# Kernel optimization log

Measured on AMD Instinct MI355X. Metric: run time of the kernel, lower is better.

## Reference

```python
import jax, jax.numpy as jnp
from jax import lax
import numpy as np

B, T, DM = 4, 2048, 768
LYR, DI, N, DC, R = 2, 1536, 64, 4, 48  # layers, d_inner, d_state, d_conv, dt_rank
EPS = 1e-5


def _silu(x):
    return x * jax.nn.sigmoid(x)


def _layernorm(x, w, b):
    m = x.mean(-1, keepdims=True)
    v = ((x - m) ** 2).mean(-1, keepdims=True)
    return (x - m) * lax.rsqrt(v + EPS) * w + b


def _mamba(x, W_in, Wc, bc, W_x, W_dt, b_dt, a_log, Dp, W_out):
    # x: [B,T,DM]; standard Mamba block (mamba_ssm), bias-free in/out projections
    b, t, _ = x.shape
    d_inner = Dp.shape[0]
    n = a_log.shape[1]
    r = W_dt.shape[1]
    xz = jnp.einsum('btd,ed->bte', x, W_in)      # [B,T,2*DI]
    u, z = jnp.split(xz, 2, axis=-1)
    # causal depthwise conv along T
    u_c = lax.conv_general_dilated(u.transpose(0, 2, 1), Wc[:, None, :], (1,),
                                   [(DC - 1, 0)], dimension_numbers=('NCH', 'OIH', 'NCH'),
                                   feature_group_count=d_inner)
    u_c = _silu((u_c + bc[None, :, None]).transpose(0, 2, 1))  # [B,T,DI]
    proj = jnp.einsum('btd,ed->bte', u_c, W_x)   # [B,T,R+2N]
    dt, Bm, Cm = proj[..., :r], proj[..., r:r + n], proj[..., r + n:]
    delta = jax.nn.softplus(jnp.einsum('btr,dr->btd', dt, W_dt) + b_dt)  # [B,T,DI]
    A = -jnp.exp(a_log)                           # [DI,N]

    def step(h, inp):
        d_t, u_t, B_t, C_t = inp                 # [B,DI],[B,DI],[B,N],[B,N]
        h = h * jnp.exp(d_t[..., None] * A) + d_t[..., None] * B_t[:, None, :] * u_t[..., None]
        return h, jnp.einsum('bdn,bn->bd', h, C_t)

    h0 = jnp.zeros((b, d_inner, n), x.dtype)
    _, ys = lax.scan(step, h0, (delta.transpose(1, 0, 2), u_c.transpose(1, 0, 2),
                                Bm.transpose(1, 0, 2), Cm.transpose(1, 0, 2)))
    y = ys.transpose(1, 0, 2) + u_c * Dp         # [B,T,DI]
    y = y * _silu(z)
    return jnp.einsum('btd,od->bto', y, W_out)   # [B,T,DM]


def setup_inputs() -> dict:
    key = jax.random.key(0)
    ks = jax.random.split(key, 12)
    s = 0.02
    A0 = jnp.log(jnp.arange(1, N + 1, dtype=jnp.float32))  # standard S4D-real init
    return {
        'x': jax.random.normal(ks[0], (B, T, DM), jnp.float32),
        'mask': jnp.ones((B, T), jnp.float32),
        'film_gamma': 1.0 + 0.1 * jax.random.normal(ks[1], (LYR, B, T, DM), jnp.float32),
        'film_beta': 0.1 * jax.random.normal(ks[2], (LYR, B, T, DM), jnp.float32),
        'in_proj_w': s * jax.random.normal(ks[3], (LYR, 2 * DI, DM), jnp.float32),
        'conv_w': s * jax.random.normal(ks[4], (LYR, DI, DC), jnp.float32),
        'conv_b': s * jax.random.normal(ks[5], (LYR, DI), jnp.float32),
        'x_proj_w': s * jax.random.normal(ks[6], (LYR, R + 2 * N, DI), jnp.float32),
        'dt_proj_w': s * jax.random.normal(ks[7], (LYR, DI, R), jnp.float32),
        'dt_proj_b': jnp.full((LYR, DI), -4.6, jnp.float32),  # softplus -> dt ~ 0.01
        'A_log': jnp.broadcast_to(A0, (LYR, DI, N)).copy(),
        'D': jnp.ones((LYR, DI), jnp.float32),
        'out_proj_w': s * jax.random.normal(ks[8], (LYR, DM, DI), jnp.float32),
        'ln_w': jnp.ones((LYR, DM), jnp.float32),
        'ln_b': jnp.zeros((LYR, DM), jnp.float32),
    }


def reference(x, mask, film_gamma, film_beta, in_proj_w, conv_w, conv_b, x_proj_w,
              dt_proj_w, dt_proj_b, A_log, D, out_proj_w, ln_w, ln_b):
    x = x * mask[..., None]
    for i in range(in_proj_w.shape[0]):
        residual = x
        h = _mamba(x, in_proj_w[i], conv_w[i], conv_b[i], x_proj_w[i], dt_proj_w[i],
                   dt_proj_b[i], A_log[i], D[i], out_proj_w[i])
        h = _layernorm(h, ln_w[i], ln_b[i])
        h = film_gamma[i] * h + film_beta[i]
        x = h + residual  # dropout is identity in eval mode
    return x
```

## Files before the change

kernel.cpp:

```cpp
#include <hip/hip_runtime.h>
#include <hip/hip_bf16.h>
#include <math.h>

#define BBv   4
#define TTv   2048
#define DMv   768
#define DIv   1536
#define NSv   64
#define DCv   4
#define RRv   48
#define PJW   176
#define NLYR  2
#define MROWS (BBv * TTv)

#define TBLK  16
#define LDST  68

typedef __attribute__((ext_vector_type(8))) short short8;
typedef __attribute__((ext_vector_type(4))) float f32x4;

__device__ __forceinline__ __hip_bfloat16 f2bf(float f) { return __float2bfloat16(f); }
__device__ __forceinline__ float bf2f(__hip_bfloat16 h) { return __bfloat162float(h); }
__device__ __forceinline__ float bits2f(unsigned u) {
    union { unsigned u; float f; } c; c.u = u; return c.f;
}

__global__ void cvt_weights_kernel(const float* __restrict__ w_in,
                                   const float* __restrict__ w_xp,
                                   const float* __restrict__ w_dt,
                                   const float* __restrict__ w_out,
                                   __hip_bfloat16* __restrict__ o_in,
                                   __hip_bfloat16* __restrict__ o_xp,
                                   __hip_bfloat16* __restrict__ o_dt,
                                   __hip_bfloat16* __restrict__ o_out)
{
    const size_t S1 = (size_t)NLYR * 2 * DIv * DMv;
    const size_t S2 = (size_t)NLYR * PJW * DIv;
    const size_t S3 = (size_t)NLYR * DIv * RRv;
    const size_t S4 = (size_t)NLYR * DMv * DIv;
    const size_t total = S1 + S2 + S3 + S4;
    for (size_t i = (size_t)blockIdx.x * blockDim.x + threadIdx.x; i < total;
         i += (size_t)gridDim.x * blockDim.x) {
        if (i < S1)                o_in[i]            = f2bf(w_in[i]);
        else if (i < S1 + S2)      o_xp[i - S1]       = f2bf(w_xp[i - S1]);
        else if (i < S1 + S2 + S3) o_dt[i - S1 - S2]  = f2bf(w_dt[i - S1 - S2]);
        else                       o_out[i - S1 - S2 - S3] = f2bf(w_out[i - S1 - S2 - S3]);
    }
}

__global__ void mask_x_kernel(const float* __restrict__ x,
                              const float* __restrict__ mask,
                              float* __restrict__ x_cur,
                              __hip_bfloat16* __restrict__ x_bf)
{
    size_t idx = (size_t)blockIdx.x * 256 + threadIdx.x;
    if (idx >= (size_t)MROWS * DMv) return;
    size_t row = idx / DMv;
    float v = x[idx] * mask[row];
    x_cur[idx] = v;
    x_bf[idx] = f2bf(v);
}

__global__ __launch_bounds__(256)
void transpose_bf16(const ushort* __restrict__ in, ushort* __restrict__ out,
                    int R, int C)
{
    __shared__ ushort s[64][68];
    const int tx = threadIdx.x & 15;
    const int ty = threadIdx.x >> 4;
    const size_t r0 = (size_t)blockIdx.y * 64;
    const size_t c0 = (size_t)blockIdx.x * 64;
    #pragma unroll
    for (int i = 0; i < 4; ++i) {
        int r = ty + 16 * i;
        ushort4 v = *(const ushort4*)(in + (r0 + r) * C + c0 + tx * 4);
        *(ushort4*)&s[r][tx * 4] = v;
    }
    __syncthreads();
    #pragma unroll
    for (int i = 0; i < 4; ++i) {
        int c = ty + 16 * i;
        ushort4 v;
        v.x = s[tx * 4 + 0][c];
        v.y = s[tx * 4 + 1][c];
        v.z = s[tx * 4 + 2][c];
        v.w = s[tx * 4 + 3][c];
        *(ushort4*)(out + (c0 + c) * R + r0 + tx * 4) = v;
    }
}

template<int EPI>
__global__ __launch_bounds__(256)
void gemm_nt(const __hip_bfloat16* __restrict__ A, int lda,
             const __hip_bfloat16* __restrict__ Bw, int ldb,
             float* __restrict__ Cf, __hip_bfloat16* __restrict__ Ch,
             __hip_bfloat16* __restrict__ ChT, int ldc,
             const float* __restrict__ bias, int M, int N, int K)
{
    __shared__ __align__(16) __hip_bfloat16 sA[64 * 48];
    __shared__ __align__(16) __hip_bfloat16 sB[64 * 48];
    const int tid = threadIdx.x;
    const int m0 = blockIdx.y * 64;
    const int n0 = blockIdx.x * 64;
    const int w = tid >> 6, lane = tid & 63;
    const int wr = (w >> 1) << 5;
    const int wc = (w & 1) << 5;
    const int lr = lane & 15, lk = lane >> 4;
    const int srow = tid >> 2;
    const int scol = (tid & 3) << 3;
    f32x4 acc[2][2] = {};
    const bool bvalid = (n0 + srow) < N;

    for (int k0 = 0; k0 < K; k0 += 32) {
        uint4 av = {0u, 0u, 0u, 0u}, bv = {0u, 0u, 0u, 0u};
        const bool kv = (k0 + scol) < K;
        if (kv)
            av = *(const uint4*)(A + (size_t)(m0 + srow) * lda + (k0 + scol));
        if (kv && bvalid)
            bv = *(const uint4*)(Bw + (size_t)(n0 + srow) * ldb + (k0 + scol));
        *(uint4*)(sA + srow * 48 + scol) = av;
        *(uint4*)(sB + srow * 48 + scol) = bv;
        __syncthreads();
        short8 af0 = *(const short8*)(sA + (wr + lr) * 48 + (lk << 3));
        short8 af1 = *(const short8*)(sA + (wr + 16 + lr) * 48 + (lk << 3));
        short8 bf0 = *(const short8*)(sB + (wc + lr) * 48 + (lk << 3));
        short8 bf1 = *(const short8*)(sB + (wc + 16 + lr) * 48 + (lk << 3));
        acc[0][0] = __builtin_amdgcn_mfma_f32_16x16x32_bf16(af0, bf0, acc[0][0], 0, 0, 0);
        acc[0][1] = __builtin_amdgcn_mfma_f32_16x16x32_bf16(af0, bf1, acc[0][1], 0, 0, 0);
        acc[1][0] = __builtin_amdgcn_mfma_f32_16x16x32_bf16(af1, bf0, acc[1][0], 0, 0, 0);
        acc[1][1] = __builtin_amdgcn_mfma_f32_16x16x32_bf16(af1, bf1, acc[1][1], 0, 0, 0);
        __syncthreads();
    }
    #pragma unroll
    for (int i = 0; i < 2; ++i) {
        #pragma unroll
        for (int j = 0; j < 2; ++j) {
            const int col = n0 + wc + (j << 4) + lr;
            const int rowb = m0 + wr + (i << 4) + (lk << 2);
            if (col >= N) continue;
            if constexpr (EPI == 0) {
                #pragma unroll
                for (int r = 0; r < 4; ++r)
                    Cf[(size_t)(rowb + r) * ldc + col] = acc[i][j][r];
            } else if constexpr (EPI == 2) {
                f32x4 sp;
                #pragma unroll
                for (int r = 0; r < 4; ++r) {
                    float xx = acc[i][j][r] + bias[col];
                    sp[r] = fmaxf(xx, 0.f) + log1pf(__expf(-fabsf(xx)));
                }
                *(f32x4*)(Cf + (size_t)col * MROWS + rowb) = sp;
            } else if constexpr (EPI == 3) {
                #pragma unroll
                for (int r = 0; r < 4; ++r) {
                    const int row = rowb + r;
                    float v = acc[i][j][r];
                    if (col < RRv)
                        Ch[(size_t)row * RRv + col] = f2bf(v);
                    else if (col < RRv + NSv)
                        Cf[(size_t)row * 128 + 2 * (col - RRv)] = v;
                    else
                        Cf[(size_t)row * 128 + 2 * (col - RRv - NSv) + 1] = v;
                }
            } else {
                if (col < DIv) {
                    #pragma unroll
                    for (int r = 0; r < 4; ++r)
                        Ch[(size_t)(rowb + r) * DIv + col] = f2bf(acc[i][j][r]);
                } else {
                    union { ushort4 v; __hip_bfloat16 h[4]; } zz;
                    #pragma unroll
                    for (int r = 0; r < 4; ++r) zz.h[r] = f2bf(acc[i][j][r]);
                    *(ushort4*)(ChT + (size_t)(col - DIv) * MROWS + rowb) = zz.v;
                }
            }
        }
    }
}

__global__ void conv_silu_kernel(const __hip_bfloat16* __restrict__ u_raw,
                                 const float* __restrict__ Wc,
                                 const float* __restrict__ bc,
                                 __hip_bfloat16* __restrict__ uc)
{
    size_t idx = (size_t)blockIdx.x * 256 + threadIdx.x;
    if (idx >= (size_t)MROWS * DIv) return;
    int d = (int)(idx % DIv);
    size_t row = idx / DIv;
    int t = (int)(row % TTv);
    float acc = bc[d];
    #pragma unroll
    for (int k = 0; k < DCv; ++k) {
        int tt = t - (DCv - 1) + k;
        if (tt >= 0)
            acc += Wc[d * DCv + k] *
                   bf2f(u_raw[(row - (DCv - 1) + k) * DIv + d]);
    }
    float s = acc / (1.f + __expf(-acc));
    uc[idx] = f2bf(s);
}

__global__ __launch_bounds__(256, 6)
void scan_kernel(const float* __restrict__ deltaT,
                 const __hip_bfloat16* __restrict__ ucT,
                 const __hip_bfloat16* __restrict__ zT,
                 const float* __restrict__ BC,
                 const float* __restrict__ a_log,
                 const float* __restrict__ Dp,
                 __hip_bfloat16* __restrict__ yT)
{
    __shared__ __align__(16) float vbuf[4 * TBLK * LDST];
    const int w = threadIdx.x >> 6;
    const int lane = threadIdx.x & 63;
    const int wid = blockIdx.x * 4 + w;
    const int b = __builtin_amdgcn_readfirstlane(wid / DIv);
    const int d = __builtin_amdgcn_readfirstlane(wid % DIv);
    const size_t bT = (size_t)b * TTv;
    const size_t dbase = (size_t)d * MROWS + bT;

    const float A2 = -__expf(a_log[(size_t)d * NSv + lane]) * 1.44269504088896f;
    const float Dd = Dp[d];

    const float4* dp4 = (const float4*)(deltaT + dbase);
    const uint4*  up4 = (const uint4*)(ucT + dbase);
    const float*  bcp = BC + bT * 128 + 2 * lane;
    float* vb = vbuf + w * (TBLK * LDST);

    float4 dA[2], dB[2];
    uint4  uu[2];
    float2 bc[2][8];

    dA[0] = dp4[0]; dB[0] = dp4[1]; uu[0] = up4[0];
    #pragma unroll
    for (int i = 0; i < 8; ++i)
        bc[0][i] = *(const float2*)(bcp + i * 128);

    float h = 0.f;
    for (int t0 = 0; t0 < TTv; t0 += TBLK) {
        #pragma unroll
        for (int q = 0; q < 2; ++q) {
            const int c = (t0 >> 3) + q;
            dA[q ^ 1] = dp4[(c + 1) * 2];
            dB[q ^ 1] = dp4[(c + 1) * 2 + 1];
            uu[q ^ 1] = up4[c + 1];
            const float* bq = bcp + (size_t)(c + 1) * 1024;
            #pragma unroll
            for (int i = 0; i < 8; ++i)
                bc[q ^ 1][i] = *(const float2*)(bq + i * 128);

            float dl[8] = { dA[q].x, dA[q].y, dA[q].z, dA[q].w,
                            dB[q].x, dB[q].y, dB[q].z, dB[q].w };
            float uf[8];
            uf[0] = bits2f(uu[q].x << 16); uf[1] = bits2f(uu[q].x & 0xffff0000u);
            uf[2] = bits2f(uu[q].y << 16); uf[3] = bits2f(uu[q].y & 0xffff0000u);
            uf[4] = bits2f(uu[q].z << 16); uf[5] = bits2f(uu[q].z & 0xffff0000u);
            uf[6] = bits2f(uu[q].w << 16); uf[7] = bits2f(uu[q].w & 0xffff0000u);

            #pragma unroll
            for (int i = 0; i < 8; ++i) {
                const float dlt = dl[i];
                const float e = exp2f(dlt * A2);
                h = fmaf(h, e, (dlt * uf[i]) * bc[q][i].x);
                vb[(q * 8 + i) * LDST + lane] = h * bc[q][i].y;
            }
        }
        __asm__ volatile("s_waitcnt lgkmcnt(0)" ::: "memory");
        const int r = lane & 15;
        const int cb = (lane >> 4) << 4;
        const float* vr = vb + r * LDST + cb;
        f32x4 a = *(const f32x4*)(vr);
        a += *(const f32x4*)(vr + 4);
        a += *(const f32x4*)(vr + 8);
        a += *(const f32x4*)(vr + 12);
        float s = a[0] + a[1] + a[2] + a[3];
        s += __shfl_xor(s, 16, 64);
        s += __shfl_xor(s, 32, 64);
        if (lane < 16) {
            const size_t g = dbase + t0 + r;
            const float u = bf2f(ucT[g]);
            const float z = bf2f(zT[g]);
            float yv = s + u * Dd;
            yv *= z / (1.f + __expf(-z));
            yT[g] = f2bf(yv);
        }
    }
}

__global__ __launch_bounds__(256)
void ln_film_res_kernel(const float* __restrict__ h,
                        const float* __restrict__ xres,
                        const float* __restrict__ lw,
                        const float* __restrict__ lb,
                        const float* __restrict__ gamma,
                        const float* __restrict__ beta,
                        float* __restrict__ xout,
                        __hip_bfloat16* __restrict__ xbf)
{
    __shared__ float sm[4];
    const int row = blockIdx.x;
    const int tid = threadIdx.x;
    const int w = tid >> 6, lane = tid & 63;
    const float* hr = h + (size_t)row * DMv;
    float v0 = hr[tid], v1 = hr[tid + 256], v2 = hr[tid + 512];

    float s = v0 + v1 + v2;
    #pragma unroll
    for (int off = 32; off > 0; off >>= 1) s += __shfl_xor(s, off, 64);
    if (lane == 0) sm[w] = s;
    __syncthreads();
    float mean = (sm[0] + sm[1] + sm[2] + sm[3]) * (1.f / DMv);
    __syncthreads();

    float d0 = v0 - mean, d1 = v1 - mean, d2 = v2 - mean;
    float vs = d0 * d0 + d1 * d1 + d2 * d2;
    #pragma unroll
    for (int off = 32; off > 0; off >>= 1) vs += __shfl_xor(vs, off, 64);
    if (lane == 0) sm[w] = vs;
    __syncthreads();
    float var = (sm[0] + sm[1] + sm[2] + sm[3]) * (1.f / DMv);
    float rstd = rsqrtf(var + 1e-5f);

    const float dv[3] = {d0, d1, d2};
    #pragma unroll
    for (int e = 0; e < 3; ++e) {
        int c = tid + e * 256;
        size_t gi = (size_t)row * DMv + c;
        float ln = dv[e] * rstd * lw[c] + lb[c];
        float f = gamma[gi] * ln + beta[gi];
        float o = f + xres[gi];
        xout[gi] = o;
        xbf[gi] = f2bf(o);
    }
}

extern "C" void kernel_launch(void* const* d_in, const int* in_sizes, int n_in,
                              void* d_out, int out_size, void* d_ws, size_t ws_size,
                              hipStream_t stream)
{
    const float* x     = (const float*)d_in[0];
    const float* mask  = (const float*)d_in[1];
    const float* fg    = (const float*)d_in[2];
    const float* fb    = (const float*)d_in[3];
    const float* w_in  = (const float*)d_in[4];
    const float* w_c   = (const float*)d_in[5];
    const float* b_c   = (const float*)d_in[6];
    const float* w_xp  = (const float*)d_in[7];
    const float* w_dt  = (const float*)d_in[8];
    const float* b_dt  = (const float*)d_in[9];
    const float* a_log = (const float*)d_in[10];
    const float* Dp    = (const float*)d_in[11];
    const float* w_out = (const float*)d_in[12];
    const float* ln_w  = (const float*)d_in[13];
    const float* ln_b  = (const float*)d_in[14];

    char* p = (char*)d_ws;
    __hip_bfloat16* uraw_yT = (__hip_bfloat16*)p; p += (size_t)MROWS * DIv * 2;
    __hip_bfloat16* uc_y    = (__hip_bfloat16*)p; p += (size_t)MROWS * DIv * 2;
    __hip_bfloat16* ucT     = (__hip_bfloat16*)p; p += (size_t)DIv * MROWS * 2 + 4096;
    __hip_bfloat16* zT      = (__hip_bfloat16*)p; p += (size_t)DIv * MROWS * 2;
    __hip_bfloat16* x_bf    = (__hip_bfloat16*)p; p += (size_t)MROWS * DMv * 2;
    __hip_bfloat16* dtA_bf  = (__hip_bfloat16*)p; p += (size_t)MROWS * RRv * 2;
    __hip_bfloat16* wbf_in  = (__hip_bfloat16*)p; p += (size_t)NLYR * 2 * DIv * DMv * 2;
    __hip_bfloat16* wbf_xp  = (__hip_bfloat16*)p; p += (size_t)NLYR * PJW * DIv * 2;
    __hip_bfloat16* wbf_dt  = (__hip_bfloat16*)p; p += (size_t)NLYR * DIv * RRv * 2;
    __hip_bfloat16* wbf_out = (__hip_bfloat16*)p; p += (size_t)NLYR * DMv * DIv * 2;
    float* BCbuf  = (float*)p; p += (size_t)MROWS * 128 * 4 + 8192;
    float* deltaT = (float*)p; p += (size_t)DIv * MROWS * 4 + 4096;
    float* x_cur  = (float*)p; p += (size_t)MROWS * DMv * 4;
    float* hbuf   = deltaT;

    cvt_weights_kernel<<<4096, 256, 0, stream>>>(w_in, w_xp, w_dt, w_out,
                                                 wbf_in, wbf_xp, wbf_dt, wbf_out);
    mask_x_kernel<<<(MROWS * DMv) / 256, 256, 0, stream>>>(x, mask, x_cur, x_bf);

    for (int L = 0; L < NLYR; ++L) {
        const __hip_bfloat16* WinL  = wbf_in  + (size_t)L * 2 * DIv * DMv;
        const __hip_bfloat16* WxpL  = wbf_xp  + (size_t)L * PJW * DIv;
        const __hip_bfloat16* WdtL  = wbf_dt  + (size_t)L * DIv * RRv;
        const __hip_bfloat16* WoutL = wbf_out + (size_t)L * DMv * DIv;

        gemm_nt<4><<<dim3(2 * DIv / 64, MROWS / 64), 256, 0, stream>>>(
            x_bf, DMv, WinL, DMv, nullptr, uraw_yT, zT, 0, nullptr,
            MROWS, 2 * DIv, DMv);

        conv_silu_kernel<<<(MROWS * DIv) / 256, 256, 0, stream>>>(
            uraw_yT, w_c + (size_t)L * DIv * DCv, b_c + (size_t)L * DIv, uc_y);

        transpose_bf16<<<dim3(DIv / 64, MROWS / 64), 256, 0, stream>>>(
            (const ushort*)uc_y, (ushort*)ucT, MROWS, DIv);

        gemm_nt<3><<<dim3((PJW + 63) / 64, MROWS / 64), 256, 0, stream>>>(
            uc_y, DIv, WxpL, DIv, BCbuf, dtA_bf, nullptr, 0, nullptr,
            MROWS, PJW, DIv);

        gemm_nt<2><<<dim3(DIv / 64, MROWS / 64), 256, 0, stream>>>(
            dtA_bf, RRv, WdtL, RRv, deltaT, nullptr, nullptr, 0,
            b_dt + (size_t)L * DIv, MROWS, DIv, RRv);

        scan_kernel<<<(BBv * DIv) / 4, 256, 0, stream>>>(
            deltaT, ucT, zT, BCbuf,
            a_log + (size_t)L * DIv * NSv, Dp + (size_t)L * DIv, uraw_yT);

        transpose_bf16<<<dim3(MROWS / 64, DIv / 64), 256, 0, stream>>>(
            (const ushort*)uraw_yT, (ushort*)uc_y, DIv, MROWS);

        gemm_nt<0><<<dim3(DMv / 64, MROWS / 64), 256, 0, stream>>>(
            uc_y, DIv, WoutL, DIv, hbuf, nullptr, nullptr, DMv, nullptr,
            MROWS, DMv, DIv);

        float* xo = (L == NLYR - 1) ? (float*)d_out : x_cur;
        ln_film_res_kernel<<<MROWS, 256, 0, stream>>>(
            hbuf, x_cur, ln_w + (size_t)L * DMv, ln_b + (size_t)L * DMv,
            fg + (size_t)L * MROWS * DMv, fb + (size_t)L * MROWS * DMv,
            xo, x_bf);
    }
}
```

Before: 1.588 ms.

## Enlarge GEMM tile to 128x64 and use hardware exp2/rcp intrinsics

The bf16 MFMA GEMM goes from a 64x64 to a 128x64 block tile. Each wave now computes 32x64 with 8 accumulators, and the LDS stride is padded to 56 to reduce bank conflicts. Operand reuse per K step is higher and fewer blocks load B. Separately, the sigmoid/SiLU and exp computations in the conv, scan init, scan recurrence and scan gating switch to the raw amdgcn exp2/rcp builtins, which cost fewer instructions but are slightly less accurate. Doubling the tile halves the grid and adds register pressure.

Result: faster. 1.553 ms (-2.2%).

```diff
diff --git a/kernel.cpp b/kernel.cpp
--- a/kernel.cpp
+++ b/kernel.cpp
@@ -16,6 +16,8 @@
 #define TBLK  16
 #define LDST  68
 
+#define GST   56
+
 typedef __attribute__((ext_vector_type(8))) short short8;
 typedef __attribute__((ext_vector_type(4))) float f32x4;
 
@@ -24,6 +26,9 @@
 __device__ __forceinline__ float bits2f(unsigned u) {
     union { unsigned u; float f; } c; c.u = u; return c.f;
 }
+#define EXP2(x) __builtin_amdgcn_exp2f(x)
+#define RCPF(x) __builtin_amdgcn_rcpf(x)
+#define LOG2E 1.44269504088896f
 
 __global__ void cvt_weights_kernel(const float* __restrict__ w_in,
                                    const float* __restrict__ w_xp,
@@ -97,45 +102,54 @@
              __hip_bfloat16* __restrict__ ChT, int ldc,
              const float* __restrict__ bias, int M, int N, int K)
 {
-    __shared__ __align__(16) __hip_bfloat16 sA[64 * 48];
-    __shared__ __align__(16) __hip_bfloat16 sB[64 * 48];
+    __shared__ __align__(16) __hip_bfloat16 sA[128 * GST];
+    __shared__ __align__(16) __hip_bfloat16 sB[64 * GST];
     const int tid = threadIdx.x;
-    const int m0 = blockIdx.y * 64;
+    const int m0 = blockIdx.y * 128;
     const int n0 = blockIdx.x * 64;
     const int w = tid >> 6, lane = tid & 63;
-    const int wr = (w >> 1) << 5;
-    const int wc = (w & 1) << 5;
+    const int wr = w << 5;
     const int lr = lane & 15, lk = lane >> 4;
-    const int srow = tid >> 2;
-    const int scol = (tid & 3) << 3;
-    f32x4 acc[2][2] = {};
-    const bool bvalid = (n0 + srow) < N;
+    const int ar = tid >> 1;
+    const int ak = (tid & 1) << 4;
+    const int br = tid >> 2;
+    const int bk = (tid & 3) << 3;
+    f32x4 acc[2][4] = {};
+    const bool bvalid = (n0 + br) < N;
 
     for (int k0 = 0; k0 < K; k0 += 32) {
-        uint4 av = {0u, 0u, 0u, 0u}, bv = {0u, 0u, 0u, 0u};
-        const bool kv = (k0 + scol) < K;
-        if (kv)
-            av = *(const uint4*)(A + (size_t)(m0 + srow) * lda + (k0 + scol));
-        if (kv && bvalid)
-            bv = *(const uint4*)(Bw + (size_t)(n0 + srow) * ldb + (k0 + scol));
-        *(uint4*)(sA + srow * 48 + scol) = av;
-        *(uint4*)(sB + srow * 48 + scol) = bv;
+        uint4 a0 = {0u,0u,0u,0u}, a1 = {0u,0u,0u,0u}, bv = {0u,0u,0u,0u};
+        if (k0 + ak < K)
+            a0 = *(const uint4*)(A + (size_t)(m0 + ar) * lda + k0 + ak);
+        if (k0 + ak + 8 < K)
+            a1 = *(const uint4*)(A + (size_t)(m0 + ar) * lda + k0 + ak + 8);
+        if (bvalid && k0 + bk < K)
+            bv = *(const uint4*)(Bw + (size_t)(n0 + br) * ldb + k0 + bk);
+        *(uint4*)(sA + ar * GST + ak) = a0;
+        *(uint4*)(sA + ar * GST + ak + 8) = a1;
+        *(uint4*)(sB + br * GST + bk) = bv;
         __syncthreads();
-        short8 af0 = *(const short8*)(sA + (wr + lr) * 48 + (lk << 3));
-        short8 af1 = *(const short8*)(sA + (wr + 16 + lr) * 48 + (lk << 3));
-        short8 bf0 = *(const short8*)(sB + (wc + lr) * 48 + (lk << 3));
-        short8 bf1 = *(const short8*)(sB + (wc + 16 + lr) * 48 + (lk << 3));
+        short8 af0 = *(const short8*)(sA + (wr + lr) * GST + (lk << 3));
+        short8 af1 = *(const short8*)(sA + (wr + 16 + lr) * GST + (lk << 3));
+        short8 bf0 = *(const short8*)(sB + (lr) * GST + (lk << 3));
+        short8 bf1 = *(const short8*)(sB + (16 + lr) * GST + (lk << 3));
+        short8 bf2 = *(const short8*)(sB + (32 + lr) * GST + (lk << 3));
+        short8 bf3 = *(const short8*)(sB + (48 + lr) * GST + (lk << 3));
         acc[0][0] = __builtin_amdgcn_mfma_f32_16x16x32_bf16(af0, bf0, acc[0][0], 0, 0, 0);
         acc[0][1] = __builtin_amdgcn_mfma_f32_16x16x32_bf16(af0, bf1, acc[0][1], 0, 0, 0);
+        acc[0][2] = __builtin_amdgcn_mfma_f32_16x16x32_bf16(af0, bf2, acc[0][2], 0, 0, 0);
+        acc[0][3] = __builtin_amdgcn_mfma_f32_16x16x32_bf16(af0, bf3, acc[0][3], 0, 0, 0);
         acc[1][0] = __builtin_amdgcn_mfma_f32_16x16x32_bf16(af1, bf0, acc[1][0], 0, 0, 0);
         acc[1][1] = __builtin_amdgcn_mfma_f32_16x16x32_bf16(af1, bf1, acc[1][1], 0, 0, 0);
+        acc[1][2] = __builtin_amdgcn_mfma_f32_16x16x32_bf16(af1, bf2, acc[1][2], 0, 0, 0);
+        acc[1][3] = __builtin_amdgcn_mfma_f32_16x16x32_bf16(af1, bf3, acc[1][3], 0, 0, 0);
         __syncthreads();
     }
     #pragma unroll
     for (int i = 0; i < 2; ++i) {
         #pragma unroll
-        for (int j = 0; j < 2; ++j) {
-            const int col = n0 + wc + (j << 4) + lr;
+        for (int j = 0; j < 4; ++j) {
+            const int col = n0 + (j << 4) + lr;
             const int rowb = m0 + wr + (i << 4) + (lk << 2);
             if (col >= N) continue;
             if constexpr (EPI == 0) {
@@ -196,7 +210,7 @@
             acc += Wc[d * DCv + k] *
                    bf2f(u_raw[(row - (DCv - 1) + k) * DIv + d]);
     }
-    float s = acc / (1.f + __expf(-acc));
+    float s = acc * RCPF(1.f + EXP2(-acc * LOG2E));
     uc[idx] = f2bf(s);
 }
 
@@ -218,7 +232,7 @@
     const size_t bT = (size_t)b * TTv;
     const size_t dbase = (size_t)d * MROWS + bT;
 
-    const float A2 = -__expf(a_log[(size_t)d * NSv + lane]) * 1.44269504088896f;
+    const float A2 = -EXP2(a_log[(size_t)d * NSv + lane] * LOG2E) * LOG2E;
     const float Dd = Dp[d];
 
     const float4* dp4 = (const float4*)(deltaT + dbase);
@@ -259,7 +273,7 @@
             #pragma unroll
             for (int i = 0; i < 8; ++i) {
                 const float dlt = dl[i];
-                const float e = exp2f(dlt * A2);
+                const float e = EXP2(dlt * A2);
                 h = fmaf(h, e, (dlt * uf[i]) * bc[q][i].x);
                 vb[(q * 8 + i) * LDST + lane] = h * bc[q][i].y;
             }
@@ -280,7 +294,7 @@
             const float u = bf2f(ucT[g]);
             const float z = bf2f(zT[g]);
             float yv = s + u * Dd;
-            yv *= z / (1.f + __expf(-z));
+            yv *= z * RCPF(1.f + EXP2(-z * LOG2E));
             yT[g] = f2bf(yv);
         }
     }
@@ -379,7 +393,7 @@
         const __hip_bfloat16* WdtL  = wbf_dt  + (size_t)L * DIv * RRv;
         const __hip_bfloat16* WoutL = wbf_out + (size_t)L * DMv * DIv;
 
-        gemm_nt<4><<<dim3(2 * DIv / 64, MROWS / 64), 256, 0, stream>>>(
+        gemm_nt<4><<<dim3(2 * DIv / 64, MROWS / 128), 256, 0, stream>>>(
             x_bf, DMv, WinL, DMv, nullptr, uraw_yT, zT, 0, nullptr,
             MROWS, 2 * DIv, DMv);
 
@@ -389,11 +403,11 @@
         transpose_bf16<<<dim3(DIv / 64, MROWS / 64), 256, 0, stream>>>(
             (const ushort*)uc_y, (ushort*)ucT, MROWS, DIv);
 
-        gemm_nt<3><<<dim3((PJW + 63) / 64, MROWS / 64), 256, 0, stream>>>(
+        gemm_nt<3><<<dim3((PJW + 63) / 64, MROWS / 128), 256, 0, stream>>>(
             uc_y, DIv, WxpL, DIv, BCbuf, dtA_bf, nullptr, 0, nullptr,
             MROWS, PJW, DIv);
 
-        gemm_nt<2><<<dim3(DIv / 64, MROWS / 64), 256, 0, stream>>>(
+        gemm_nt<2><<<dim3(DIv / 64, MROWS / 128), 256, 0, stream>>>(
             dtA_bf, RRv, WdtL, RRv, deltaT, nullptr, nullptr, 0,
             b_dt + (size_t)L * DIv, MROWS, DIv, RRv);
 
@@ -404,7 +418,7 @@
         transpose_bf16<<<dim3(MROWS / 64, DIv / 64), 256, 0, stream>>>(
             (const ushort*)uraw_yT, (ushort*)uc_y, DIv, MROWS);
 
-        gemm_nt<0><<<dim3(DMv / 64, MROWS / 64), 256, 0, stream>>>(
+        gemm_nt<0><<<dim3(DMv / 64, MROWS / 128), 256, 0, stream>>>(
             uc_y, DIv, WoutL, DIv, hbuf, nullptr, nullptr, DMv, nullptr,
             MROWS, DMv, DIv);
 
```
